# Kernel tuning notes

Hardware: AMD Instinct MI355X
Metric: run time of the kernel (lower is better)

The kernel has to match this reference:

```python
import jax, jax.numpy as jnp
import numpy as np

B_NW, N, DIM, NH, DH, HID, NW, WH = 2048, 64, 512, 16, 32, 384, 64, 8
EPS = 1e-12  # F.normalize eps

def _rel_coords_log(wh, ww):
    # torch.cartesian_prod order: i (rows) outer, j (cols) inner
    ii, jj = np.meshgrid(np.arange(wh), np.arange(ww), indexing='ij')
    coords = np.stack([ii.ravel(), jj.ravel()], axis=-1).astype(np.float32)  # [N,2]
    rel = coords[:, None, :] - coords[None, :, :]                            # [N,N,2]
    return (np.sign(rel) * np.log1p(np.abs(rel))).astype(np.float32)

def setup_inputs() -> dict:
    key = jax.random.key(0)
    ks = jax.random.split(key, 9)
    s = 0.02
    inner = NH * DH
    return {
        'x': jax.random.normal(ks[0], (B_NW, N, DIM), jnp.float32),
        'mask': jax.random.normal(ks[1], (NW, N, N), jnp.float32),
        'w_qkv': jax.random.normal(ks[2], (DIM, 3 * inner), jnp.float32) * s,
        'tau': jnp.ones((1, NH, 1, 1), jnp.float32),
        'mlp_w1': jax.random.normal(ks[3], (2, HID), jnp.float32) * s,
        'mlp_b1': jnp.zeros((HID,), jnp.float32),
        'mlp_w2': jax.random.normal(ks[4], (HID, NH), jnp.float32) * s,
        'mlp_b2': jnp.zeros((NH,), jnp.float32),
        'w_out': jax.random.normal(ks[5], (inner, DIM), jnp.float32) * s,
        'b_out': jnp.zeros((DIM,), jnp.float32),
        'rel_log': jnp.asarray(_rel_coords_log(WH, WH)),
    }

def reference(x, mask, w_qkv, tau, mlp_w1, mlp_b1, mlp_w2, mlp_b2, w_out, b_out, rel_log):
    b, n, _ = x.shape
    qkv = x @ w_qkv                                   # [b, n, 3*nh*dh]
    qkv = qkv.reshape(b, n, 3, NH, DH)
    q, k, v = (jnp.transpose(qkv[:, :, i], (0, 2, 1, 3)) for i in range(3))  # [b, nh, n, dh]
    # cosine attention: L2-normalize q and k along head dim
    q = q / jnp.maximum(jnp.linalg.norm(q, axis=-1, keepdims=True), EPS)
    k = k / jnp.maximum(jnp.linalg.norm(k, axis=-1, keepdims=True), EPS)
    sim = jnp.einsum('bhid,bhjd->bhij', q, k) * tau   # learned temperature
    # relative position bias via meta MLP: [N,N,2] -> [N,N,nh]
    bias = jax.nn.relu(rel_log @ mlp_w1 + mlp_b1) @ mlp_w2 + mlp_b2
    sim = sim + jnp.transpose(bias, (2, 0, 1))[None]  # [1, nh, N, N]
    nw = mask.shape[0]
    sim = sim.reshape(b // nw, nw, NH, n, n) + mask[None, :, None]
    sim = sim.reshape(b, NH, n, n)
    attn = jax.nn.softmax(sim, axis=-1)
    out = jnp.einsum('bhij,bhjd->bhid', attn, v)
    out = jnp.transpose(out, (0, 2, 1, 3)).reshape(b, n, NH * DH)
    return out @ w_out + b_out
```

## Files before the change

### kernel.cpp

```cpp
#include <hip/hip_runtime.h>
#include <hip/hip_bf16.h>


typedef __bf16 bf16;
typedef __bf16 v2bf __attribute__((ext_vector_type(2)));
typedef __bf16 v4bf __attribute__((ext_vector_type(4)));
typedef __bf16 v8bf __attribute__((ext_vector_type(8)));
typedef float  v4f  __attribute__((ext_vector_type(4)));

#define AS1 __attribute__((address_space(1)))
#define AS3 __attribute__((address_space(3)))

__device__ __forceinline__ int swzA(int o) { return o ^ (((o >> 10) & 7) << 4); }
__device__ __forceinline__ int swzB(int o) { return o ^ (((o >> 7) & 3) << 4); }

__device__ __forceinline__ unsigned packbf(float a, float b) {
    v2bf t = { (bf16)a, (bf16)b };
    return __builtin_bit_cast(unsigned, t);
}

__global__ void convert_w_kernel(const float* __restrict__ wqkv, const float* __restrict__ wout,
                                 bf16* __restrict__ Wt, bf16* __restrict__ WoT) {
    int idx = blockIdx.x * 256 + threadIdx.x;
    Wt[idx] = (bf16)wqkv[(idx & 511) * 1536 + (idx >> 9)];
    if (idx < 262144) WoT[idx] = (bf16)wout[(idx & 511) * 512 + (idx >> 9)];
}

__global__ void bias_kernel(const float* __restrict__ rel_log, const float* __restrict__ w1,
                            const float* __restrict__ b1, const float* __restrict__ w2,
                            const float* __restrict__ b2, float* __restrict__ bias) {
    int p = blockIdx.x * 256 + threadIdx.x;
    float ra = rel_log[p * 2 + 0];
    float rb = rel_log[p * 2 + 1];
    float acc[16];
    #pragma unroll
    for (int t = 0; t < 16; ++t) acc[t] = 0.f;
    for (int kk = 0; kk < 384; ++kk) {
        float hv = fmaxf(ra * w1[kk] + rb * w1[384 + kk] + b1[kk], 0.f);
        #pragma unroll
        for (int t = 0; t < 16; ++t) acc[t] += hv * w2[kk * 16 + t];
    }
    #pragma unroll
    for (int t = 0; t < 16; ++t) bias[t * 4096 + p] = acc[t] + b2[t];
}

__global__ void comb_kernel(const float* __restrict__ bias, const float* __restrict__ mask,
                            float* __restrict__ comb) {
    int idx = blockIdx.x * 256 + threadIdx.x;
    int t = idx & 4095, wh = idx >> 12;
    int w = wh >> 4, h = wh & 15;
    int ji = t >> 8, rem = t & 255;
    int j = ji >> 2, i = ji & 3;
    int q16 = rem >> 2, r = t & 3;
    int lq = q16 >> 4, lm = q16 & 15;
    int p = (i * 16 + lm) * 64 + j * 16 + lq * 4 + r;
    comb[idx] = bias[h * 4096 + p] + mask[w * 4096 + p];
}

__global__ __launch_bounds__(512, 1) void qkv_fused_kernel(
    const float* __restrict__ x,
    const bf16* __restrict__ Wt,
    bf16* __restrict__ q_ws, bf16* __restrict__ k_ws, bf16* __restrict__ v_ws)
{
    __shared__ alignas(16) char Albuf[65536];
    __shared__ alignas(16) char Blbuf[8][2][4096];
    const int mb = blockIdx.x;
    const int t = threadIdx.x;
    const int wv = t >> 6, lane = t & 63, lq = lane >> 4, lm = lane & 15;

    {
        const char* xbase = (const char*)x + (size_t)mb * 64 * 2048;
        #pragma unroll
        for (int p = 0; p < 8; ++p) {
            int o = p * 8192 + t * 16;
            const float4* src = (const float4*)(xbase + (size_t)o * 2);
            float4 f0 = src[0], f1 = src[1];
            v8bf a = { (bf16)f0.x, (bf16)f0.y, (bf16)f0.z, (bf16)f0.w,
                       (bf16)f1.x, (bf16)f1.y, (bf16)f1.z, (bf16)f1.w };
            *(v8bf*)(&Albuf[swzA(o)]) = a;
        }
    }

    auto stageB = [&](int buf, int pass, int kt) {
        const char* bBase = (const char*)Wt + (size_t)(pass * 512 + wv * 64) * 1024;
        char* dst = &Blbuf[wv][buf][0];
        #pragma unroll
        for (int p = 0; p < 4; ++p) {
            int o = p * 1024 + lane * 16;
            int s = swzB(o);
            __builtin_amdgcn_global_load_lds(
                (const AS1 void*)(bBase + (size_t)(s >> 6) * 1024 + kt * 64 + (s & 63)),
                (AS3 void*)(dst + o), 16, 0, 0);
        }
    };

    stageB(0, 0, 0);
    __syncthreads();

    int abase[4], boff[4];
    #pragma unroll
    for (int i = 0; i < 4; ++i) {
        int arow = i * 16 + lm;
        abase[i] = (arow * 1024 + lq * 16) ^ ((arow & 7) << 4);
        int brow = i * 16 + lm;
        boff[i] = (brow * 64) + (((lq ^ (brow >> 1)) & 3) * 16);
    }

    const int bw = mb;
    v4f acc[4][4];
    #pragma unroll
    for (int i = 0; i < 4; ++i)
        #pragma unroll
        for (int j = 0; j < 4; ++j) acc[i][j] = v4f{0.f, 0.f, 0.f, 0.f};

    #pragma unroll 1
    for (int ph = 0; ph < 48; ++ph) {
        const int pass = ph >> 4, kt = ph & 15;
        if (ph < 47) {
            const int nph = ph + 1;
            stageB(nph & 1, nph >> 4, nph & 15);
            asm volatile("s_waitcnt vmcnt(4)" ::: "memory");
        } else {
            asm volatile("s_waitcnt vmcnt(0)" ::: "memory");
        }
        __builtin_amdgcn_sched_barrier(0);
        const char* Bb = &Blbuf[wv][ph & 1][0];
        v8bf af[4], bfj[4];
        #pragma unroll
        for (int j = 0; j < 4; ++j) bfj[j] = *(const v8bf*)(Bb + boff[j]);
        #pragma unroll
        for (int i = 0; i < 4; ++i) af[i] = *(const v8bf*)(&Albuf[abase[i] ^ (kt << 6)]);
        #pragma unroll
        for (int i = 0; i < 4; ++i)
            #pragma unroll
            for (int j = 0; j < 4; ++j)
                acc[i][j] = __builtin_amdgcn_mfma_f32_16x16x32_bf16(af[i], bfj[j], acc[i][j], 0, 0, 0);

        if (kt == 15) {
            if (pass < 2) {
                bf16* dst = (pass == 0) ? q_ws : k_ws;
                #pragma unroll
                for (int j = 0; j < 4; ++j) {
                    const int h = wv * 2 + (j >> 1);
                    const int dcol = (j & 1) * 16 + lm;
                    #pragma unroll
                    for (int i = 0; i < 4; ++i)
                        #pragma unroll
                        for (int r = 0; r < 4; ++r) {
                            int n = i * 16 + lq * 4 + r;
                            dst[((size_t)(bw * 16 + h) * 64 + n) * 32 + dcol] = (bf16)acc[i][j][r];
                        }
                }
            } else {
                #pragma unroll
                for (int j = 0; j < 4; ++j) {
                    const int h = wv * 2 + (j >> 1);
                    const int dh = (j & 1) * 16 + lm;
                    #pragma unroll
                    for (int i = 0; i < 4; ++i) {
                        v4bf pv = { (bf16)acc[i][j][0], (bf16)acc[i][j][1],
                                    (bf16)acc[i][j][2], (bf16)acc[i][j][3] };
                        *(v4bf*)(v_ws + ((size_t)(bw * 16 + h) * 32 + dh) * 64 + i * 16 + lq * 4) = pv;
                    }
                }
            }
            #pragma unroll
            for (int i = 0; i < 4; ++i)
                #pragma unroll
                for (int j = 0; j < 4; ++j) acc[i][j] = v4f{0.f, 0.f, 0.f, 0.f};
        }
    }
}

__global__ __launch_bounds__(512, 4) void attn_proj_kernel(
    const bf16* __restrict__ q_ws,
    const bf16* __restrict__ k_ws,
    const bf16* __restrict__ v_ws,
    const float* __restrict__ comb,
    const float* __restrict__ tau,
    const bf16* __restrict__ WoT,
    const float* __restrict__ b_out,
    int wofs,
    float* __restrict__ out)
{
    __shared__ alignas(16) bf16 AO[64 * 520];
    const int b = blockIdx.x;
    const int tid = threadIdx.x;
    const int wv = tid >> 6, lane = tid & 63, lq = lane >> 4, lm = lane & 15;
    const v4f z4 = {0.f, 0.f, 0.f, 0.f};
    const int src0 = ((lq & 1) * 2) * 16 + lm;
    const int src1 = src0 + 16;
    const bool hisel = (lq >> 1) != 0;

    #pragma unroll 1
    for (int hh = 0; hh < 2; ++hh) {
        const int h = wv * 2 + hh;
        const size_t qk_base = (size_t)(b * 16 + h) * 64 * 32;
        const float* comb_hw = comb + ((size_t)(((wofs + b) & 63) * 16 + h)) * 4096
                                    + (lq * 16 + lm) * 4;
        const float tau_h = tau[h];

        v8bf qf[4], kf[4];
        #pragma unroll
        for (int i = 0; i < 4; ++i)
            qf[i] = *(const v8bf*)(q_ws + qk_base + (i * 16 + lm) * 32 + lq * 8);
        #pragma unroll
        for (int j = 0; j < 4; ++j)
            kf[j] = *(const v8bf*)(k_ws + qk_base + (j * 16 + lm) * 32 + lq * 8);

        #pragma unroll
        for (int i = 0; i < 4; ++i) {
            float a = 0.f;
            #pragma unroll
            for (int e = 0; e < 8; ++e) { float f = (float)qf[i][e]; a = fmaf(f, f, a); }
            a += __shfl_xor(a, 16); a += __shfl_xor(a, 32);
            float sc = tau_h / fmaxf(sqrtf(a), 1e-12f);
            #pragma unroll
            for (int e = 0; e < 8; ++e) qf[i][e] = (bf16)((float)qf[i][e] * sc);
        }
        #pragma unroll
        for (int j = 0; j < 4; ++j) {
            float a = 0.f;
            #pragma unroll
            for (int e = 0; e < 8; ++e) { float f = (float)kf[j][e]; a = fmaf(f, f, a); }
            a += __shfl_xor(a, 16); a += __shfl_xor(a, 32);
            float sc = 1.0f / fmaxf(sqrtf(a), 1e-12f);
            #pragma unroll
            for (int e = 0; e < 8; ++e) kf[j][e] = (bf16)((float)kf[j][e] * sc);
        }

        v4f st[4][4];
        #pragma unroll
        for (int j = 0; j < 4; ++j)
            #pragma unroll
            for (int i = 0; i < 4; ++i)
                st[j][i] = __builtin_amdgcn_mfma_f32_16x16x32_bf16(kf[j], qf[i], z4, 0, 0, 0);

        #pragma unroll
        for (int j = 0; j < 4; ++j)
            #pragma unroll
            for (int i = 0; i < 4; ++i) {
                float4 cv = *(const float4*)(comb_hw + (j * 4 + i) * 256);
                st[j][i][0] += cv.x; st[j][i][1] += cv.y;
                st[j][i][2] += cv.z; st[j][i][3] += cv.w;
            }

        unsigned p_lo[4][4], p_hi[4][4];
        #pragma unroll
        for (int i = 0; i < 4; ++i) {
            float mx = st[0][i][0];
            #pragma unroll
            for (int j = 0; j < 4; ++j)
                #pragma unroll
                for (int r = 0; r < 4; ++r) mx = fmaxf(mx, st[j][i][r]);
            mx = fmaxf(mx, __shfl_xor(mx, 16));
            mx = fmaxf(mx, __shfl_xor(mx, 32));
            float sm = 0.f;
            #pragma unroll
            for (int j = 0; j < 4; ++j)
                #pragma unroll
                for (int r = 0; r < 4; ++r) {
                    float e = __expf(st[j][i][r] - mx);
                    st[j][i][r] = e; sm += e;
                }
            sm += __shfl_xor(sm, 16); sm += __shfl_xor(sm, 32);
            float rcp = 1.0f / sm;
            #pragma unroll
            for (int j = 0; j < 4; ++j) {
                p_lo[j][i] = packbf(st[j][i][0] * rcp, st[j][i][1] * rcp);
                p_hi[j][i] = packbf(st[j][i][2] * rcp, st[j][i][3] * rcp);
            }
        }

        const size_t v_base = (size_t)(b * 16 + h) * 32 * 64;
        v4f o[4][2];
        #pragma unroll
        for (int i = 0; i < 4; ++i)
            #pragma unroll
            for (int nt = 0; nt < 2; ++nt) o[i][nt] = z4;
        #pragma unroll
        for (int kk = 0; kk < 2; ++kk) {
            v8bf vf[2];
            #pragma unroll
            for (int nt = 0; nt < 2; ++nt)
                vf[nt] = *(const v8bf*)(v_ws + v_base + (nt * 16 + lm) * 64 + kk * 32 + lq * 8);
            #pragma unroll
            for (int i = 0; i < 4; ++i) {
                unsigned a0 = __shfl((int)p_lo[2 * kk][i], src0);
                unsigned b0 = __shfl((int)p_lo[2 * kk + 1][i], src0);
                unsigned a1 = __shfl((int)p_hi[2 * kk][i], src0);
                unsigned b1 = __shfl((int)p_hi[2 * kk + 1][i], src0);
                unsigned a2 = __shfl((int)p_lo[2 * kk][i], src1);
                unsigned b2 = __shfl((int)p_lo[2 * kk + 1][i], src1);
                unsigned a3 = __shfl((int)p_hi[2 * kk][i], src1);
                unsigned b3 = __shfl((int)p_hi[2 * kk + 1][i], src1);
                union { unsigned u[4]; v8bf v; } c;
                c.u[0] = hisel ? b0 : a0;
                c.u[1] = hisel ? b1 : a1;
                c.u[2] = hisel ? b2 : a2;
                c.u[3] = hisel ? b3 : a3;
                v8bf pf = c.v;
                #pragma unroll
                for (int nt = 0; nt < 2; ++nt)
                    o[i][nt] = __builtin_amdgcn_mfma_f32_16x16x32_bf16(pf, vf[nt], o[i][nt], 0, 0, 0);
            }
        }
        #pragma unroll
        for (int i = 0; i < 4; ++i)
            #pragma unroll
            for (int nt = 0; nt < 2; ++nt)
                #pragma unroll
                for (int r = 0; r < 4; ++r)
                    AO[(i * 16 + lq * 4 + r) * 520 + h * 32 + nt * 16 + lm] = (bf16)o[i][nt][r];
    }

    __syncthreads();

    v4f acc[4][4];
    #pragma unroll
    for (int i = 0; i < 4; ++i)
        #pragma unroll
        for (int j = 0; j < 4; ++j) acc[i][j] = v4f{0.f, 0.f, 0.f, 0.f};

    #pragma unroll 2
    for (int kc = 0; kc < 16; ++kc) {
        v8bf af[4], bfj[4];
        #pragma unroll
        for (int j = 0; j < 4; ++j)
            bfj[j] = *(const v8bf*)(WoT + (size_t)(wv * 64 + j * 16 + lm) * 512 + kc * 32 + lq * 8);
        #pragma unroll
        for (int i = 0; i < 4; ++i)
            af[i] = *(const v8bf*)(AO + (i * 16 + lm) * 520 + kc * 32 + lq * 8);
        #pragma unroll
        for (int i = 0; i < 4; ++i)
            #pragma unroll
            for (int j = 0; j < 4; ++j)
                acc[i][j] = __builtin_amdgcn_mfma_f32_16x16x32_bf16(af[i], bfj[j], acc[i][j], 0, 0, 0);
    }

    #pragma unroll
    for (int j = 0; j < 4; ++j) {
        const int col = wv * 64 + j * 16 + lm;
        const float bo = b_out[col];
        #pragma unroll
        for (int i = 0; i < 4; ++i)
            #pragma unroll
            for (int r = 0; r < 4; ++r)
                out[(size_t)(b * 64 + i * 16 + lq * 4 + r) * 512 + col] = acc[i][j][r] + bo;
    }
}

extern "C" void kernel_launch(void* const* d_in, const int* in_sizes, int n_in,
                              void* d_out, int out_size, void* d_ws, size_t ws_size,
                              hipStream_t stream) {
    (void)in_sizes; (void)n_in; (void)out_size;
    const float* x       = (const float*)d_in[0];
    const float* mask    = (const float*)d_in[1];
    const float* w_qkv   = (const float*)d_in[2];
    const float* tau     = (const float*)d_in[3];
    const float* mlp_w1  = (const float*)d_in[4];
    const float* mlp_b1  = (const float*)d_in[5];
    const float* mlp_w2  = (const float*)d_in[6];
    const float* mlp_b2  = (const float*)d_in[7];
    const float* w_out   = (const float*)d_in[8];
    const float* b_out   = (const float*)d_in[9];
    const float* rel_log = (const float*)d_in[10];
    float* out = (float*)d_out;

    char* ws = (char*)d_ws;
    bf16*  Wt     = (bf16*)(ws);
    bf16*  WoT    = (bf16*)(ws + 1572864);
    float* bias   = (float*)(ws + 2097152);
    float* comb   = (float*)(ws + 2359296);
    char*  qkv_base = ws + 19136512;

    size_t avail = (ws_size > 19136512ULL) ? ws_size - 19136512ULL : 0;
    int W = 2048;
    while (W > 128 && (size_t)W * 196608ULL > avail) W >>= 1;
    const size_t qkbuf = (size_t)W * 65536;
    bf16* qb = (bf16*)qkv_base;
    bf16* kb = (bf16*)(qkv_base + qkbuf);
    bf16* vb = (bf16*)(qkv_base + 2 * qkbuf);

    convert_w_kernel<<<3072, 256, 0, stream>>>(w_qkv, w_out, Wt, WoT);
    bias_kernel<<<16, 256, 0, stream>>>(rel_log, mlp_w1, mlp_b1, mlp_w2, mlp_b2, bias);
    comb_kernel<<<16384, 256, 0, stream>>>(bias, mask, comb);

    const int nchunk = 2048 / W;
    for (int c = 0; c < nchunk; ++c) {
        const float* xc = x + (size_t)c * W * 64 * 512;
        qkv_fused_kernel<<<W, 512, 0, stream>>>(xc, Wt, qb, kb, vb);
        attn_proj_kernel<<<W, 512, 0, stream>>>(qb, kb, vb, comb, tau, WoT, b_out,
                                                c * W, out + (size_t)c * W * 64 * 512);
    }
}
```

Measured before the change: 683.6 us.

## Split QKV B-operand staging between LDS and direct register loads per k-pair

The QKV GEMM now consumes two k-tiles per phase. One B tile is staged into LDS through global_load_lds, and the other is loaded straight from global memory into registers and double-buffered across phases. This halves the number of loop iterations and LDS staging steps and removes the per-iteration kt==15 branch. The first B stage is also issued before the x-to-bf16 conversion so it overlaps that prologue. In exchange it uses more registers and more uncoalesced global loads from Wt, which may hurt with launch_bounds(512,1).

```diff
diff --git a/kernel.cpp b/kernel.cpp
--- a/kernel.cpp
+++ b/kernel.cpp
@@ -65,21 +65,8 @@
     __shared__ alignas(16) char Albuf[65536];
     __shared__ alignas(16) char Blbuf[8][2][4096];
     const int mb = blockIdx.x;
-    const int t = threadIdx.x;
-    const int wv = t >> 6, lane = t & 63, lq = lane >> 4, lm = lane & 15;
-
-    {
-        const char* xbase = (const char*)x + (size_t)mb * 64 * 2048;
-        #pragma unroll
-        for (int p = 0; p < 8; ++p) {
-            int o = p * 8192 + t * 16;
-            const float4* src = (const float4*)(xbase + (size_t)o * 2);
-            float4 f0 = src[0], f1 = src[1];
-            v8bf a = { (bf16)f0.x, (bf16)f0.y, (bf16)f0.z, (bf16)f0.w,
-                       (bf16)f1.x, (bf16)f1.y, (bf16)f1.z, (bf16)f1.w };
-            *(v8bf*)(&Albuf[swzA(o)]) = a;
-        }
-    }
+    const int t0 = threadIdx.x;
+    const int wv = t0 >> 6, lane = t0 & 63, lq = lane >> 4, lm = lane & 15;
 
     auto stageB = [&](int buf, int pass, int kt) {
         const char* bBase = (const char*)Wt + (size_t)(pass * 512 + wv * 64) * 1024;
@@ -93,8 +80,29 @@
                 (AS3 void*)(dst + o), 16, 0, 0);
         }
     };
-
+    auto loadRegB = [&](v8bf (&r)[4], int pass, int kt) {
+        const bf16* bBase = Wt + (size_t)(pass * 512 + wv * 64) * 512;
+        #pragma unroll
+        for (int j = 0; j < 4; ++j)
+            r[j] = *(const v8bf*)(bBase + (size_t)(j * 16 + lm) * 512 + kt * 32 + lq * 8);
+    };
+
+    v8bf rA[4], rB[4];
     stageB(0, 0, 0);
+    loadRegB(rA, 0, 1);
+
+    {
+        const char* xbase = (const char*)x + (size_t)mb * 64 * 2048;
+        #pragma unroll
+        for (int p = 0; p < 8; ++p) {
+            int o = p * 8192 + t0 * 16;
+            const float4* src = (const float4*)(xbase + (size_t)o * 2);
+            float4 f0 = src[0], f1 = src[1];
+            v8bf a = { (bf16)f0.x, (bf16)f0.y, (bf16)f0.z, (bf16)f0.w,
+                       (bf16)f1.x, (bf16)f1.y, (bf16)f1.z, (bf16)f1.w };
+            *(v8bf*)(&Albuf[swzA(o)]) = a;
+        }
+    }
     __syncthreads();
 
     int abase[4], boff[4];
@@ -113,62 +121,77 @@
         #pragma unroll
         for (int j = 0; j < 4; ++j) acc[i][j] = v4f{0.f, 0.f, 0.f, 0.f};
 
-    #pragma unroll 1
-    for (int ph = 0; ph < 48; ++ph) {
-        const int pass = ph >> 4, kt = ph & 15;
-        if (ph < 47) {
-            const int nph = ph + 1;
-            stageB(nph & 1, nph >> 4, nph & 15);
-            asm volatile("s_waitcnt vmcnt(4)" ::: "memory");
+    auto phase = [&](int pass, int t, v8bf (&ruse)[4], v8bf (&rload)[4]) {
+        const bool last = (pass == 2) && (t == 7);
+        if (!last) {
+            const int np = (t == 7) ? pass + 1 : pass;
+            const int nL = (t == 7) ? 0 : 2 * (t + 1);
+            stageB((t + 1) & 1, np, nL);
+            loadRegB(rload, np, nL + 1);
+            asm volatile("s_waitcnt vmcnt(8)" ::: "memory");
         } else {
             asm volatile("s_waitcnt vmcnt(0)" ::: "memory");
         }
         __builtin_amdgcn_sched_barrier(0);
-        const char* Bb = &Blbuf[wv][ph & 1][0];
-        v8bf af[4], bfj[4];
-        #pragma unroll
-        for (int j = 0; j < 4; ++j) bfj[j] = *(const v8bf*)(Bb + boff[j]);
-        #pragma unroll
-        for (int i = 0; i < 4; ++i) af[i] = *(const v8bf*)(&Albuf[abase[i] ^ (kt << 6)]);
+        const char* Bb = &Blbuf[wv][t & 1][0];
+        const int ktL = 2 * t, ktR = 2 * t + 1;
+        v8bf bL[4], afL[4], afR[4];
+        #pragma unroll
+        for (int j = 0; j < 4; ++j) bL[j] = *(const v8bf*)(Bb + boff[j]);
+        #pragma unroll
+        for (int i = 0; i < 4; ++i) afL[i] = *(const v8bf*)(&Albuf[abase[i] ^ (ktL << 6)]);
+        #pragma unroll
+        for (int i = 0; i < 4; ++i) afR[i] = *(const v8bf*)(&Albuf[abase[i] ^ (ktR << 6)]);
         #pragma unroll
         for (int i = 0; i < 4; ++i)
             #pragma unroll
             for (int j = 0; j < 4; ++j)
-                acc[i][j] = __builtin_amdgcn_mfma_f32_16x16x32_bf16(af[i], bfj[j], acc[i][j], 0, 0, 0);
-
-        if (kt == 15) {
-            if (pass < 2) {
-                bf16* dst = (pass == 0) ? q_ws : k_ws;
-                #pragma unroll
-                for (int j = 0; j < 4; ++j) {
-                    const int h = wv * 2 + (j >> 1);
-                    const int dcol = (j & 1) * 16 + lm;
+                acc[i][j] = __builtin_amdgcn_mfma_f32_16x16x32_bf16(afL[i], bL[j], acc[i][j], 0, 0, 0);
+        #pragma unroll
+        for (int i = 0; i < 4; ++i)
+            #pragma unroll
+            for (int j = 0; j < 4; ++j)
+                acc[i][j] = __builtin_amdgcn_mfma_f32_16x16x32_bf16(afR[i], ruse[j], acc[i][j], 0, 0, 0);
+    };
+
+    #pragma unroll 1
+    for (int pass = 0; pass < 3; ++pass) {
+        #pragma unroll
+        for (int t = 0; t < 8; ++t) {
+            if ((t & 1) == 0) phase(pass, t, rA, rB);
+            else              phase(pass, t, rB, rA);
+        }
+        if (pass < 2) {
+            bf16* dst = (pass == 0) ? q_ws : k_ws;
+            #pragma unroll
+            for (int j = 0; j < 4; ++j) {
+                const int h = wv * 2 + (j >> 1);
+                const int dcol = (j & 1) * 16 + lm;
+                #pragma unroll
+                for (int i = 0; i < 4; ++i)
                     #pragma unroll
-                    for (int i = 0; i < 4; ++i)
-                        #pragma unroll
-                        for (int r = 0; r < 4; ++r) {
-                            int n = i * 16 + lq * 4 + r;
-                            dst[((size_t)(bw * 16 + h) * 64 + n) * 32 + dcol] = (bf16)acc[i][j][r];
-                        }
-                }
-            } else {
-                #pragma unroll
-                for (int j = 0; j < 4; ++j) {
-                    const int h = wv * 2 + (j >> 1);
-                    const int dh = (j & 1) * 16 + lm;
-                    #pragma unroll
-                    for (int i = 0; i < 4; ++i) {
-                        v4bf pv = { (bf16)acc[i][j][0], (bf16)acc[i][j][1],
-                                    (bf16)acc[i][j][2], (bf16)acc[i][j][3] };
-                        *(v4bf*)(v_ws + ((size_t)(bw * 16 + h) * 32 + dh) * 64 + i * 16 + lq * 4) = pv;
+                    for (int r = 0; r < 4; ++r) {
+                        int n = i * 16 + lq * 4 + r;
+                        dst[((size_t)(bw * 16 + h) * 64 + n) * 32 + dcol] = (bf16)acc[i][j][r];
                     }
+            }
+        } else {
+            #pragma unroll
+            for (int j = 0; j < 4; ++j) {
+                const int h = wv * 2 + (j >> 1);
+                const int dh = (j & 1) * 16 + lm;
+                #pragma unroll
+                for (int i = 0; i < 4; ++i) {
+                    v4bf pv = { (bf16)acc[i][j][0], (bf16)acc[i][j][1],
+                                (bf16)acc[i][j][2], (bf16)acc[i][j][3] };
+                    *(v4bf*)(v_ws + ((size_t)(bw * 16 + h) * 32 + dh) * 64 + i * 16 + lq * 4) = pv;
                 }
             }
-            #pragma unroll
-            for (int i = 0; i < 4; ++i)
-                #pragma unroll
-                for (int j = 0; j < 4; ++j) acc[i][j] = v4f{0.f, 0.f, 0.f, 0.f};
-        }
+        }
+        #pragma unroll
+        for (int i = 0; i < 4; ++i)
+            #pragma unroll
+            for (int j = 0; j < 4; ++j) acc[i][j] = v4f{0.f, 0.f, 0.f, 0.f};
     }
 }
 
```

Result: no change. 683.7 us (+0.0%).
